# Kernel optimization log

Measured on AMD Instinct MI355X. Metric: run time of the kernel, lower is better.

The kernel has to match this reference:

```python
import jax, jax.numpy as jnp
import numpy as np
import math

SIZE = 11
PAD = 5
C1 = 0.01 ** 2
C2 = 0.03 ** 2


def gaussian_window():
    # Matches torch __init__: 1D gaussian (sigma=1.5), normalized, outer product,
    # expanded to depthwise weight of shape (3, 1, 11, 11)
    x = np.arange(SIZE, dtype=np.float32)
    g = np.exp(-((x - SIZE // 2) ** 2) / (2.0 * 1.5 ** 2)).astype(np.float32)
    g = g / g.sum()
    w2d = np.outer(g, g).astype(np.float32)  # (11, 11)
    return jnp.asarray(np.broadcast_to(w2d, (3, 1, SIZE, SIZE)).copy())


def depthwise_conv(x, win):
    return jax.lax.conv_general_dilated(
        x, win,
        window_strides=(1, 1),
        padding=[(PAD, PAD), (PAD, PAD)],
        dimension_numbers=('NCHW', 'OIHW', 'NCHW'),
        feature_group_count=3,
    )


def setup_inputs() -> dict:
    key = jax.random.key(0)
    k1, k2 = jax.random.split(key)
    img1 = jax.random.uniform(k1, (16, 3, 512, 512), dtype=jnp.float32)
    img2 = jax.random.uniform(k2, (16, 3, 512, 512), dtype=jnp.float32)
    return {"img1": img1, "img2": img2, "win": gaussian_window()}


def reference(img1, img2, win):
    mu1 = depthwise_conv(img1, win)
    mu2 = depthwise_conv(img2, win)
    mu1_sq = mu1 * mu1
    mu2_sq = mu2 * mu2
    mu1_mu2 = mu1 * mu2
    sig1_sq = depthwise_conv(img1 * img1, win) - mu1_sq
    sig2_sq = depthwise_conv(img2 * img2, win) - mu2_sq
    sig12 = depthwise_conv(img1 * img2, win) - mu1_mu2
    v = ((2.0 * mu1_mu2 + C1) * (2.0 * sig12 + C2)) / (
        (mu1_sq + mu2_sq + C1) * (sig1_sq + sig2_sq + C2))
    return 1.0 - jnp.mean(v)
```

## Files before the change

### kernel.cpp

```cpp
#include <hip/hip_runtime.h>


#define IMG 512
#define NPIX (16LL * 3 * 512 * 512)
#define NBLK (16 * 16 * 48)
#define RP 56
#define HP 56

typedef short v8s __attribute__((ext_vector_type(8)));
typedef float v4f __attribute__((ext_vector_type(4)));
typedef __bf16 bf2 __attribute__((ext_vector_type(2)));
typedef float f2  __attribute__((ext_vector_type(2)));

__device__ __forceinline__ int cvtpk(float lo, float hi) {
    f2 f; f.x = lo; f.y = hi;
    bf2 r = __builtin_convertvector(f, bf2);
    return __builtin_bit_cast(int, r);
}
__device__ __forceinline__ unsigned f2bf(float f) {
    unsigned u = __float_as_uint(f);
    return (u + 0x7FFFu + ((u >> 16) & 1u)) >> 16;
}

template <bool EDGE>
__device__ __forceinline__ void stage_tile(
    const float* __restrict__ p1, const float* __restrict__ p2,
    int tx0, int ty0, int tid, short (*raw)[48][RP])
{
    for (int idx = tid; idx < 48 * 6; idx += 256) {
        const int row = idx / 6;
        const int grp = idx - row * 6;
        const int gr  = ty0 - 8 + row;
        const int gc  = tx0 - 8 + grp * 8;
        float4 a0, a1, b0, b1;
        if (!EDGE) {
            const size_t o = (size_t)gr * IMG + gc;
            a0 = *(const float4*)(p1 + o);
            a1 = *(const float4*)(p1 + o + 4);
            b0 = *(const float4*)(p2 + o);
            b1 = *(const float4*)(p2 + o + 4);
        } else {
            float4 z; z.x = z.y = z.z = z.w = 0.f;
            a0 = a1 = b0 = b1 = z;
            if ((unsigned)gr < IMG) {
                const float* r1 = p1 + (size_t)gr * IMG;
                const float* r2 = p2 + (size_t)gr * IMG;
                if ((unsigned)gc < IMG)       { a0 = *(const float4*)(r1 + gc);     b0 = *(const float4*)(r2 + gc); }
                if ((unsigned)(gc + 4) < IMG) { a1 = *(const float4*)(r1 + gc + 4); b1 = *(const float4*)(r2 + gc + 4); }
            }
        }
        const int c = grp * 8;
        int4 w;
        w.x = cvtpk(a0.x, a0.y); w.y = cvtpk(a0.z, a0.w);
        w.z = cvtpk(a1.x, a1.y); w.w = cvtpk(a1.z, a1.w);
        *(int4*)&raw[0][row][c] = w;
        w.x = cvtpk(b0.x, b0.y); w.y = cvtpk(b0.z, b0.w);
        w.z = cvtpk(b1.x, b1.y); w.w = cvtpk(b1.z, b1.w);
        *(int4*)&raw[1][row][c] = w;
        w.x = cvtpk(fmaf(a0.x, a0.x, b0.x * b0.x), fmaf(a0.y, a0.y, b0.y * b0.y));
        w.y = cvtpk(fmaf(a0.z, a0.z, b0.z * b0.z), fmaf(a0.w, a0.w, b0.w * b0.w));
        w.z = cvtpk(fmaf(a1.x, a1.x, b1.x * b1.x), fmaf(a1.y, a1.y, b1.y * b1.y));
        w.w = cvtpk(fmaf(a1.z, a1.z, b1.z * b1.z), fmaf(a1.w, a1.w, b1.w * b1.w));
        *(int4*)&raw[2][row][c] = w;
        w.x = cvtpk(a0.x * b0.x, a0.y * b0.y);
        w.y = cvtpk(a0.z * b0.z, a0.w * b0.w);
        w.z = cvtpk(a1.x * b1.x, a1.y * b1.y);
        w.w = cvtpk(a1.z * b1.z, a1.w * b1.w);
        *(int4*)&raw[3][row][c] = w;
    }
}

__global__ __launch_bounds__(256, 4) void ssim_kernel(
    const float* __restrict__ img1,
    const float* __restrict__ img2,
    const float* __restrict__ win,
    float* __restrict__ partial)
{
    __shared__ __align__(16) short raw [4][48][RP];
    __shared__ __align__(16) short hbuf[4][32][HP];
    __shared__ float sg[12];
    __shared__ float red[4];

    const int tid  = threadIdx.x;
    const int lane = tid & 63;
    const int wave = tid >> 6;
    const int lm   = lane & 15;
    const int quad = lane >> 4;

    const int bx = blockIdx.x, by = blockIdx.y, z = blockIdx.z;
    const int tx0 = bx * 32, ty0 = by * 32;

    if (tid < 12) sg[tid] = (tid < 11) ? win[55 + tid] * rsqrtf(win[60]) : 0.f;

    const size_t zoff = (size_t)z * IMG * IMG;
    const float* p1 = img1 + zoff;
    const float* p2 = img2 + zoff;

    const bool edge = (bx == 0) | (bx == 15) | (by == 0) | (by == 15);
    if (!edge) stage_tile<false>(p1, p2, tx0, ty0, tid, raw);
    else       stage_tile<true >(p1, p2, tx0, ty0, tid, raw);
    __syncthreads();

    v8s band;
    #pragma unroll
    for (int j = 0; j < 8; ++j) {
        int t  = quad * 8 + j - lm - 3;
        int tc = ((unsigned)t > 10u) ? 11 : t;
        band[j] = (short)f2bf(sg[tc]);
    }

    const v4f zacc = {0.f, 0.f, 0.f, 0.f};
    #pragma unroll
    for (int i = 0; i < 6; ++i) {
        const int id    = wave * 6 + i;
        const int plane = id & 3;
        const int s     = id >> 2;
        const int r0    = (s < 3 ? s : s - 3) * 16;
        const int c0    = (s < 3 ? 0 : 16);
        const v8s a = *(const v8s*)&raw[plane][r0 + lm][c0 + quad * 8];
        const v4f acc = __builtin_amdgcn_mfma_f32_16x16x32_bf16(a, band, zacc, 0, 0, 0);
        int2 w2;
        w2.x = cvtpk(acc[0], acc[1]);
        w2.y = cvtpk(acc[2], acc[3]);
        *(int2*)&hbuf[plane][c0 + lm][r0 + quad * 4] = w2;
    }
    __syncthreads();

    const int r0v = (wave & 1) * 16;
    const int c0v = (wave >> 1) * 16;
    v4f acc[4];
    #pragma unroll
    for (int p = 0; p < 4; ++p) {
        const v8s hf = *(const v8s*)&hbuf[p][c0v + lm][r0v + quad * 8];
        acc[p] = __builtin_amdgcn_mfma_f32_16x16x32_bf16(band, hf, zacc, 0, 0, 0);
    }

    const float C1c = 1e-4f;
    const float C2c = 9e-4f;
    float vsum = 0.f;
    #pragma unroll
    for (int r = 0; r < 4; ++r) {
        const float m1 = acc[0][r], m2 = acc[1][r];
        const float es = acc[2][r], ex = acc[3][r];
        const float m1s = m1 * m1, m2s = m2 * m2, m12 = m1 * m2;
        const float sig = es - m1s - m2s;
        const float s12 = ex - m12;
        const float num = (2.f * m12 + C1c) * (2.f * s12 + C2c);
        const float den = (m1s + m2s + C1c) * (sig + C2c);
        vsum += num * __builtin_amdgcn_rcpf(den);
    }

    #pragma unroll
    for (int off = 32; off > 0; off >>= 1)
        vsum += __shfl_down(vsum, off, 64);
    if (lane == 0) red[wave] = vsum;
    __syncthreads();
    if (tid == 0) {
        const int bidx = (z * (int)gridDim.y + by) * (int)gridDim.x + bx;
        partial[bidx] = red[0] + red[1] + red[2] + red[3];
    }
}

__global__ __launch_bounds__(256) void finalize_kernel(
    const float* __restrict__ partial, float* __restrict__ out)
{
    __shared__ float red[4];
    const float4* p4 = (const float4*)partial;
    float s = 0.f;
    for (int i = threadIdx.x; i < NBLK / 4; i += 256) {
        float4 t = p4[i];
        s += (t.x + t.y) + (t.z + t.w);
    }
    #pragma unroll
    for (int off = 32; off > 0; off >>= 1)
        s += __shfl_down(s, off, 64);
    if ((threadIdx.x & 63) == 0) red[threadIdx.x >> 6] = s;
    __syncthreads();
    if (threadIdx.x == 0)
        out[0] = 1.0f - (red[0] + red[1] + red[2] + red[3]) / (float)NPIX;
}

extern "C" void kernel_launch(void* const* d_in, const int* in_sizes, int n_in,
                              void* d_out, int out_size, void* d_ws, size_t ws_size,
                              hipStream_t stream) {
    const float* img1 = (const float*)d_in[0];
    const float* img2 = (const float*)d_in[1];
    const float* win  = (const float*)d_in[2];
    float* partialb = (float*)d_ws;

    dim3 grid(IMG / 32, IMG / 32, 48);
    ssim_kernel<<<grid, dim3(256), 0, stream>>>(img1, img2, win, partialb);
    finalize_kernel<<<1, dim3(256), 0, stream>>>(partialb, (float*)d_out);
}
```

Baseline: 151.3 us.

## Feed horizontal MFMA directly from global loads and widen tiles to 64x32

The horizontal Gaussian pass now loads each wave's input fragment straight from global memory into registers and feeds the MFMA directly, removing the raw LDS staging buffer and one barrier. Output tiles grow from 32x32 to 64x32, so each wave owns a 16-column strip and the vertical pass runs two row tiles per wave. This lowers the halo re-read overhead and LDS traffic. The band weights are now built with a lane shuffle instead of shared memory, and the finalize reduction uses 512 threads. The trade-off is that each wave's per-lane global loads span 16 separate rows, which may coalesce less well than the old row-contiguous staging.

```diff
diff --git a/kernel.cpp b/kernel.cpp
--- a/kernel.cpp
+++ b/kernel.cpp
@@ -3,8 +3,7 @@
 
 #define IMG 512
 #define NPIX (16LL * 3 * 512 * 512)
-#define NBLK (16 * 16 * 48)
-#define RP 56
+#define NBLK (8 * 16 * 48)
 #define HP 56
 
 typedef short v8s __attribute__((ext_vector_type(8)));
@@ -23,62 +22,75 @@
 }
 
 template <bool EDGE>
-__device__ __forceinline__ void stage_tile(
+__device__ __forceinline__ void hpass(
     const float* __restrict__ p1, const float* __restrict__ p2,
-    int tx0, int ty0, int tid, short (*raw)[48][RP])
+    int tx0, int ty0, int lm, int quad, int ct, v8s band,
+    short (*hbuf)[64][HP])
 {
-    for (int idx = tid; idx < 48 * 6; idx += 256) {
-        const int row = idx / 6;
-        const int grp = idx - row * 6;
-        const int gr  = ty0 - 8 + row;
-        const int gc  = tx0 - 8 + grp * 8;
+    const v4f zacc = {0.f, 0.f, 0.f, 0.f};
+    #pragma unroll
+    for (int rt = 0; rt < 3; ++rt) {
+        const int grow = ty0 - 8 + rt * 16 + lm;
+        const int gcol = tx0 - 8 + ct * 16 + quad * 8;
         float4 a0, a1, b0, b1;
         if (!EDGE) {
-            const size_t o = (size_t)gr * IMG + gc;
-            a0 = *(const float4*)(p1 + o);
-            a1 = *(const float4*)(p1 + o + 4);
-            b0 = *(const float4*)(p2 + o);
-            b1 = *(const float4*)(p2 + o + 4);
+            const float* r1 = p1 + (size_t)grow * IMG + gcol;
+            const float* r2 = p2 + (size_t)grow * IMG + gcol;
+            a0 = *(const float4*)r1;       a1 = *(const float4*)(r1 + 4);
+            b0 = *(const float4*)r2;       b1 = *(const float4*)(r2 + 4);
         } else {
-            float4 z; z.x = z.y = z.z = z.w = 0.f;
-            a0 = a1 = b0 = b1 = z;
-            if ((unsigned)gr < IMG) {
-                const float* r1 = p1 + (size_t)gr * IMG;
-                const float* r2 = p2 + (size_t)gr * IMG;
-                if ((unsigned)gc < IMG)       { a0 = *(const float4*)(r1 + gc);     b0 = *(const float4*)(r2 + gc); }
-                if ((unsigned)(gc + 4) < IMG) { a1 = *(const float4*)(r1 + gc + 4); b1 = *(const float4*)(r2 + gc + 4); }
+            float4 z4; z4.x = z4.y = z4.z = z4.w = 0.f;
+            a0 = a1 = b0 = b1 = z4;
+            if ((unsigned)grow < IMG) {
+                const float* r1 = p1 + (size_t)grow * IMG;
+                const float* r2 = p2 + (size_t)grow * IMG;
+                if ((unsigned)gcol < IMG) {
+                    a0 = *(const float4*)(r1 + gcol);
+                    b0 = *(const float4*)(r2 + gcol);
+                }
+                if ((unsigned)(gcol + 4) < IMG) {
+                    a1 = *(const float4*)(r1 + gcol + 4);
+                    b1 = *(const float4*)(r2 + gcol + 4);
+                }
             }
         }
-        const int c = grp * 8;
+        v8s A[4];
         int4 w;
         w.x = cvtpk(a0.x, a0.y); w.y = cvtpk(a0.z, a0.w);
         w.z = cvtpk(a1.x, a1.y); w.w = cvtpk(a1.z, a1.w);
-        *(int4*)&raw[0][row][c] = w;
+        A[0] = __builtin_bit_cast(v8s, w);
         w.x = cvtpk(b0.x, b0.y); w.y = cvtpk(b0.z, b0.w);
         w.z = cvtpk(b1.x, b1.y); w.w = cvtpk(b1.z, b1.w);
-        *(int4*)&raw[1][row][c] = w;
+        A[1] = __builtin_bit_cast(v8s, w);
         w.x = cvtpk(fmaf(a0.x, a0.x, b0.x * b0.x), fmaf(a0.y, a0.y, b0.y * b0.y));
         w.y = cvtpk(fmaf(a0.z, a0.z, b0.z * b0.z), fmaf(a0.w, a0.w, b0.w * b0.w));
         w.z = cvtpk(fmaf(a1.x, a1.x, b1.x * b1.x), fmaf(a1.y, a1.y, b1.y * b1.y));
         w.w = cvtpk(fmaf(a1.z, a1.z, b1.z * b1.z), fmaf(a1.w, a1.w, b1.w * b1.w));
-        *(int4*)&raw[2][row][c] = w;
+        A[2] = __builtin_bit_cast(v8s, w);
         w.x = cvtpk(a0.x * b0.x, a0.y * b0.y);
         w.y = cvtpk(a0.z * b0.z, a0.w * b0.w);
         w.z = cvtpk(a1.x * b1.x, a1.y * b1.y);
         w.w = cvtpk(a1.z * b1.z, a1.w * b1.w);
-        *(int4*)&raw[3][row][c] = w;
+        A[3] = __builtin_bit_cast(v8s, w);
+
+        #pragma unroll
+        for (int p = 0; p < 4; ++p) {
+            const v4f acc = __builtin_amdgcn_mfma_f32_16x16x32_bf16(A[p], band, zacc, 0, 0, 0);
+            int2 w2;
+            w2.x = cvtpk(acc[0], acc[1]);
+            w2.y = cvtpk(acc[2], acc[3]);
+            *(int2*)&hbuf[p][ct * 16 + lm][rt * 16 + quad * 4] = w2;
+        }
     }
 }
 
-__global__ __launch_bounds__(256, 4) void ssim_kernel(
+__global__ __launch_bounds__(256, 5) void ssim_kernel(
     const float* __restrict__ img1,
     const float* __restrict__ img2,
     const float* __restrict__ win,
     float* __restrict__ partial)
 {
-    __shared__ __align__(16) short raw [4][48][RP];
-    __shared__ __align__(16) short hbuf[4][32][HP];
-    __shared__ float sg[12];
+    __shared__ __align__(16) short hbuf[4][64][HP];
     __shared__ float red[4];
 
     const int tid  = threadIdx.x;
@@ -88,66 +100,52 @@
     const int quad = lane >> 4;
 
     const int bx = blockIdx.x, by = blockIdx.y, z = blockIdx.z;
-    const int tx0 = bx * 32, ty0 = by * 32;
+    const int tx0 = bx * 64, ty0 = by * 32;
 
-    if (tid < 12) sg[tid] = (tid < 11) ? win[55 + tid] * rsqrtf(win[60]) : 0.f;
+    float gl = 0.f;
+    if (lane < 11) gl = win[55 + lane] * rsqrtf(win[60]);
+    v8s band;
+    #pragma unroll
+    for (int j = 0; j < 8; ++j) {
+        const int t  = quad * 8 + j - lm - 3;
+        const int tc = ((unsigned)t > 10u) ? 11 : t;
+        band[j] = (short)f2bf(__shfl(gl, tc));
+    }
 
     const size_t zoff = (size_t)z * IMG * IMG;
     const float* p1 = img1 + zoff;
     const float* p2 = img2 + zoff;
 
-    const bool edge = (bx == 0) | (bx == 15) | (by == 0) | (by == 15);
-    if (!edge) stage_tile<false>(p1, p2, tx0, ty0, tid, raw);
-    else       stage_tile<true >(p1, p2, tx0, ty0, tid, raw);
+    const bool interior = (bx > 0) & (bx < 7) & (by > 0) & (by < 15);
+    if (interior) hpass<false>(p1, p2, tx0, ty0, lm, quad, wave, band, hbuf);
+    else          hpass<true >(p1, p2, tx0, ty0, lm, quad, wave, band, hbuf);
     __syncthreads();
 
-    v8s band;
-    #pragma unroll
-    for (int j = 0; j < 8; ++j) {
-        int t  = quad * 8 + j - lm - 3;
-        int tc = ((unsigned)t > 10u) ? 11 : t;
-        band[j] = (short)f2bf(sg[tc]);
-    }
-
     const v4f zacc = {0.f, 0.f, 0.f, 0.f};
-    #pragma unroll
-    for (int i = 0; i < 6; ++i) {
-        const int id    = wave * 6 + i;
-        const int plane = id & 3;
-        const int s     = id >> 2;
-        const int r0    = (s < 3 ? s : s - 3) * 16;
-        const int c0    = (s < 3 ? 0 : 16);
-        const v8s a = *(const v8s*)&raw[plane][r0 + lm][c0 + quad * 8];
-        const v4f acc = __builtin_amdgcn_mfma_f32_16x16x32_bf16(a, band, zacc, 0, 0, 0);
-        int2 w2;
-        w2.x = cvtpk(acc[0], acc[1]);
-        w2.y = cvtpk(acc[2], acc[3]);
-        *(int2*)&hbuf[plane][c0 + lm][r0 + quad * 4] = w2;
-    }
-    __syncthreads();
-
-    const int r0v = (wave & 1) * 16;
-    const int c0v = (wave >> 1) * 16;
-    v4f acc[4];
-    #pragma unroll
-    for (int p = 0; p < 4; ++p) {
-        const v8s hf = *(const v8s*)&hbuf[p][c0v + lm][r0v + quad * 8];
-        acc[p] = __builtin_amdgcn_mfma_f32_16x16x32_bf16(band, hf, zacc, 0, 0, 0);
-    }
-
     const float C1c = 1e-4f;
     const float C2c = 9e-4f;
+    const int c0v = wave * 16;
     float vsum = 0.f;
     #pragma unroll
-    for (int r = 0; r < 4; ++r) {
-        const float m1 = acc[0][r], m2 = acc[1][r];
-        const float es = acc[2][r], ex = acc[3][r];
-        const float m1s = m1 * m1, m2s = m2 * m2, m12 = m1 * m2;
-        const float sig = es - m1s - m2s;
-        const float s12 = ex - m12;
-        const float num = (2.f * m12 + C1c) * (2.f * s12 + C2c);
-        const float den = (m1s + m2s + C1c) * (sig + C2c);
-        vsum += num * __builtin_amdgcn_rcpf(den);
+    for (int t2 = 0; t2 < 2; ++t2) {
+        const int r0v = t2 * 16;
+        v4f acc[4];
+        #pragma unroll
+        for (int p = 0; p < 4; ++p) {
+            const v8s hf = *(const v8s*)&hbuf[p][c0v + lm][r0v + quad * 8];
+            acc[p] = __builtin_amdgcn_mfma_f32_16x16x32_bf16(band, hf, zacc, 0, 0, 0);
+        }
+        #pragma unroll
+        for (int r = 0; r < 4; ++r) {
+            const float m1 = acc[0][r], m2 = acc[1][r];
+            const float es = acc[2][r], ex = acc[3][r];
+            const float m1s = m1 * m1, m2s = m2 * m2, m12 = m1 * m2;
+            const float sig = es - m1s - m2s;
+            const float s12 = ex - m12;
+            const float num = (2.f * m12 + C1c) * (2.f * s12 + C2c);
+            const float den = (m1s + m2s + C1c) * (sig + C2c);
+            vsum += num * __builtin_amdgcn_rcpf(den);
+        }
     }
 
     #pragma unroll
@@ -161,13 +159,13 @@
     }
 }
 
-__global__ __launch_bounds__(256) void finalize_kernel(
+__global__ __launch_bounds__(512) void finalize_kernel(
     const float* __restrict__ partial, float* __restrict__ out)
 {
-    __shared__ float red[4];
+    __shared__ float red[8];
     const float4* p4 = (const float4*)partial;
     float s = 0.f;
-    for (int i = threadIdx.x; i < NBLK / 4; i += 256) {
+    for (int i = threadIdx.x; i < NBLK / 4; i += 512) {
         float4 t = p4[i];
         s += (t.x + t.y) + (t.z + t.w);
     }
@@ -176,8 +174,12 @@
         s += __shfl_down(s, off, 64);
     if ((threadIdx.x & 63) == 0) red[threadIdx.x >> 6] = s;
     __syncthreads();
-    if (threadIdx.x == 0)
-        out[0] = 1.0f - (red[0] + red[1] + red[2] + red[3]) / (float)NPIX;
+    if (threadIdx.x == 0) {
+        float t = 0.f;
+        #pragma unroll
+        for (int i = 0; i < 8; ++i) t += red[i];
+        out[0] = 1.0f - t / (float)NPIX;
+    }
 }
 
 extern "C" void kernel_launch(void* const* d_in, const int* in_sizes, int n_in,
@@ -188,7 +190,7 @@
     const float* win  = (const float*)d_in[2];
     float* partialb = (float*)d_ws;
 
-    dim3 grid(IMG / 32, IMG / 32, 48);
+    dim3 grid(IMG / 64, IMG / 32, 48);
     ssim_kernel<<<grid, dim3(256), 0, stream>>>(img1, img2, win, partialb);
-    finalize_kernel<<<1, dim3(256), 0, stream>>>(partialb, (float*)d_out);
+    finalize_kernel<<<1, dim3(512), 0, stream>>>(partialb, (float*)d_out);
 }
```

Result: faster. 143.7 us (-5.0%).
